# Kernel optimization log

Measured on AMD Instinct MI355X. Metric: run time of the kernel, lower is better.

The kernel has to match this reference:

```python
import jax, jax.numpy as jnp
import numpy as np


def setup_inputs() -> dict:
    key = jax.random.key(0)
    ks = jax.random.split(key, 7)
    N, C, sy, sx = 1024, 384, 7, 7
    Dm, Dc = 64, 64
    Dg = C + Dm + Dc  # 512, must match f_t_global
    return {
        "f_t_global": jax.random.normal(ks[0], (N, Dg), dtype=jnp.float32),
        "x_t_local": jax.random.normal(ks[1], (N, C, sy, sx), dtype=jnp.float32),
        "x_t_prev_local": jax.random.normal(ks[2], (N, C, sy, sx), dtype=jnp.float32),
        "m_t": jax.random.normal(ks[3], (N, Dm), dtype=jnp.float32),
        "m_t_prev": jax.random.normal(ks[4], (N, Dm), dtype=jnp.float32),
        "c_t": jax.random.normal(ks[5], (N, Dc), dtype=jnp.float32),
        "c_t_prev": jax.random.normal(ks[6], (N, Dc), dtype=jnp.float32),
    }


def _join(loc, m, c):
    # loc: [S, N, C]; m: [N, Dm]; c: [N, Dc] -> [S, N, C+Dm+Dc]
    S, N, _ = loc.shape
    mc = jnp.concatenate([m, c], axis=-1)  # [N, Dm+Dc]
    mc = jnp.broadcast_to(mc[None], (S, N, mc.shape[-1]))
    return jnp.concatenate([loc, mc], axis=-1)


def _mean_ce_diag(logits):
    # logits: [S, N, N]; labels = arange(N) for every s -> mean over s of CE
    logp = jax.nn.log_softmax(logits, axis=-1)
    diag = jnp.diagonal(logp, axis1=1, axis2=2)  # [S, N]
    return -jnp.mean(diag)  # mean over N (per-step CE) and over S (the /(sx*sy))


def reference(f_t_global, x_t_local, x_t_prev_local, m_t, m_t_prev, c_t, c_t_prev):
    N, C, sy, sx = x_t_prev_local.shape
    S = sy * sx
    # [N,C,sy,sx] -> [S,N,C] (spatial locations batched)
    prev = x_t_prev_local.reshape(N, C, S).transpose(2, 0, 1)
    cur = x_t_local.reshape(N, C, S).transpose(2, 0, 1)
    pos = _join(prev, m_t_prev, c_t_prev)   # [S, N, D]
    # loss1: global features vs per-location previous positives
    logits1 = jnp.einsum('id,sjd->sij', f_t_global, pos)  # [S, N, N]
    loss1 = _mean_ce_diag(logits1)
    # loss2: per-location current predictions vs previous positives
    pred2 = _join(cur, m_t, c_t)            # [S, N, D]
    logits2 = jnp.einsum('sid,sjd->sij', pred2, pos)
    loss2 = _mean_ce_diag(logits2)
    loss = loss1 + loss2
    return (loss, x_t_prev_local, x_t_local)
```

## Files before the change

kernel.cpp:

```cpp
#include <hip/hip_runtime.h>
#include <hip/hip_bf16.h>

typedef __attribute__((ext_vector_type(8))) __bf16 bf16x8;
typedef __attribute__((ext_vector_type(4))) float  f32x4;

#define SDIM 49
#define NDIM 1024
#define CDIM 384
#define DDIM 512
#define DMC  64
#define SCALE (1.0f/(SDIM*NDIM))
#define SLOT 65536

__device__ __forceinline__ void gload16(const void* g, void* l) {
    __builtin_amdgcn_global_load_lds((const __attribute__((address_space(1))) void*)g,
                                     (__attribute__((address_space(3))) void*)l, 16, 0, 0);
}

__global__ __launch_bounds__(512) void pack_copy_kernel(
    const float* __restrict__ xloc, const float* __restrict__ mv,
    const float* __restrict__ cv,   __hip_bfloat16* __restrict__ dst,
    float* __restrict__ cpy)
{
    const int j = blockIdx.x;
    const int d = threadIdx.x;
    float vals[SDIM];
    if (d < CDIM) {
        const float* p = xloc + ((size_t)j * CDIM + d) * SDIM;
        #pragma unroll
        for (int s = 0; s < SDIM; ++s) vals[s] = p[s];
        float* dcp = cpy + ((size_t)j * CDIM + d) * SDIM;
        #pragma unroll
        for (int s = 0; s < SDIM; ++s) dcp[s] = vals[s];
    } else if (d < CDIM + DMC) {
        float v = mv[j * DMC + (d - CDIM)];
        #pragma unroll
        for (int s = 0; s < SDIM; ++s) vals[s] = v;
    } else {
        float v = cv[j * DMC + (d - CDIM - DMC)];
        #pragma unroll
        for (int s = 0; s < SDIM; ++s) vals[s] = v;
    }
    #pragma unroll
    for (int s = 0; s < SDIM; ++s)
        dst[((size_t)s * NDIM + j) * DDIM + d] = __float2bfloat16(vals[s]);
}

__global__ void fpack_kernel(const float* __restrict__ f,
                             __hip_bfloat16* __restrict__ dst, int n)
{
    int i = blockIdx.x * blockDim.x + threadIdx.x;
    if (i < n) dst[i] = __float2bfloat16(f[i]);
}

__global__ __launch_bounds__(512, 2) void loss_kernel(
    const __hip_bfloat16* __restrict__ Fm,
    const __hip_bfloat16* __restrict__ Km,
    const __hip_bfloat16* __restrict__ Qm,
    float2* __restrict__ part,
    float* __restrict__ out)
{
    extern __shared__ __attribute__((aligned(16))) char sm[];

    const int bid = blockIdx.x;
    const int xcd = bid & 7;
    const int jj  = bid >> 3;
    const int g0  = 196 * xcd;
    const int gend = g0 + 196;

    const int tid  = threadIdx.x;
    const int lane = tid & 63;
    const int w    = tid >> 6;
    const int l15  = lane & 15;
    const int l4   = lane >> 4;
    const int wk   = w >> 2;
    const int wq   = w & 3;

    const int trow = tid >> 3;
    const int scol = (((tid & 7) ^ ((tid >> 3) & 7)) << 4);

    const unsigned xo   = (unsigned)((l15 & 7) << 4);
    const unsigned arow = (unsigned)((wk * 128 + l15) * 128);
    const unsigned brow = 32768u + (unsigned)((wq * 64 + l15) * 128);

    auto APtr = [&](int g) -> const char* {
        const int s = g >> 5, kb = (g >> 3) & 3;
        return (const char*)Km + ((size_t)s * NDIM + (size_t)kb * 256) * 1024;
    };
    auto BPtr = [&](int g) -> const char* {
        const int s = g >> 5, qb = g & 7;
        return (qb < 4)
            ? ((const char*)Fm + (size_t)qb * 256 * 1024)
            : ((const char*)Qm + ((size_t)s * NDIM + (size_t)(qb - 4) * 256) * 1024);
    };
    auto stage8 = [&](const char* A, const char* B, int ko, char* slot) {
        #pragma unroll
        for (int c = 0; c < 4; ++c) {
            gload16(A + (size_t)(c * 64 + trow) * 1024 + ko + scol,
                    slot + c * 8192 + tid * 16);
            gload16(B + (size_t)(c * 64 + trow) * 1024 + ko + scol,
                    slot + 32768 + c * 8192 + tid * 16);
        }
    };

    f32x4 acc[8][4];
    bf16x8 afr[8], bfr[4];

    #define READ12(KC) do {                                                   \
        const unsigned co = ((unsigned)((KC) * 64 + l4 * 16)) ^ xo;           \
        _Pragma("unroll")                                                     \
        for (int a = 0; a < 8; ++a)                                           \
            afr[a] = *(const bf16x8*)(sb_ + arow + a * 2048u + co);           \
        _Pragma("unroll")                                                     \
        for (int b = 0; b < 4; ++b)                                           \
            bfr[b] = *(const bf16x8*)(sb_ + brow + b * 2048u + co);           \
    } while (0)

    #define MFMA32() do {                                                     \
        _Pragma("unroll")                                                     \
        for (int a = 0; a < 8; ++a)                                           \
            _Pragma("unroll")                                                 \
            for (int b = 0; b < 4; ++b)                                       \
                acc[a][b] = __builtin_amdgcn_mfma_f32_16x16x32_bf16(          \
                    afr[a], bfr[b], acc[a][b], 0, 0, 0);                      \
    } while (0)

    stage8(APtr(g0 + jj), BPtr(g0 + jj), 0, sm);

    for (int g = g0 + jj; g < gend; g += 32) {
        const char* Ag = APtr(g);
        const char* Bg = BPtr(g);
        const bool hasNext = (g + 32) < gend;
        const char* An = hasNext ? APtr(g + 32) : Ag;
        const char* Bn = hasNext ? BPtr(g + 32) : Bg;

        #pragma unroll
        for (int a = 0; a < 8; ++a)
            #pragma unroll
            for (int b = 0; b < 4; ++b) acc[a][b] = f32x4{0.f, 0.f, 0.f, 0.f};

        #pragma unroll
        for (int t = 0; t < 8; ++t) {
            const char* sb_ = sm + (size_t)(t & 1) * SLOT;
            char* ns_ = sm + (size_t)((t + 1) & 1) * SLOT;

            __syncthreads();

            if ((t < 7) || hasNext) {
                const char* sA = (t < 7) ? Ag : An;
                const char* sB = (t < 7) ? Bg : Bn;
                stage8(sA, sB, (t < 7) ? (t + 1) * 128 : 0, ns_);
            }
            __builtin_amdgcn_sched_barrier(0);

            READ12(0);
            __builtin_amdgcn_s_setprio(1); MFMA32(); __builtin_amdgcn_s_setprio(0);
            READ12(1);
            __builtin_amdgcn_s_setprio(1); MFMA32(); __builtin_amdgcn_s_setprio(0);
        }

        const int s  = g >> 5;
        const int kb = (g >> 3) & 3;
        const int qb = g & 7;

        float q_m[4], q_s[4];
        #pragma unroll
        for (int b = 0; b < 4; ++b) {
            float m = -3.0e38f;
            #pragma unroll
            for (int a = 0; a < 8; ++a)
                #pragma unroll
                for (int r = 0; r < 4; ++r) m = fmaxf(m, acc[a][b][r]);
            float ss = 0.0f;
            #pragma unroll
            for (int a = 0; a < 8; ++a)
                #pragma unroll
                for (int r = 0; r < 4; ++r) ss += __expf(acc[a][b][r] - m);
            #pragma unroll
            for (int off = 16; off <= 32; off <<= 1) {
                float mo = __shfl_xor(m, off, 64);
                float so = __shfl_xor(ss, off, 64);
                float nm = fmaxf(m, mo);
                ss = ss * __expf(m - nm) + so * __expf(mo - nm);
                m = nm;
            }
            q_m[b] = m; q_s[b] = ss;
        }
        if (lane < 16) {
            const size_t rowb = (size_t)s * 2048 + (size_t)qb * 256 + wq * 64 + lane;
            #pragma unroll
            for (int b = 0; b < 4; ++b)
                part[(rowb + b * 16) * 8 + kb * 2 + wk] = make_float2(q_m[b], q_s[b]);
        }

        if (kb == (qb & 3) && (wq >> 1) == wk) {
            float d = 0.0f;
            const bool lok = (((lane >> 2) & 3) == l4);
            if (wq & 1) {
                #pragma unroll
                for (int b = 0; b < 4; ++b)
                    #pragma unroll
                    for (int r = 0; r < 4; ++r)
                        if (lok && r == (lane & 3)) d += acc[4 + b][b][r];
            } else {
                #pragma unroll
                for (int b = 0; b < 4; ++b)
                    #pragma unroll
                    for (int r = 0; r < 4; ++r)
                        if (lok && r == (lane & 3)) d += acc[b][b][r];
            }
            #pragma unroll
            for (int off = 1; off < 64; off <<= 1) d += __shfl_xor(d, off, 64);
            if (lane == 0) atomicAdd(out, -d * SCALE);
        }
    }
    #undef READ12
    #undef MFMA32
}

__global__ __launch_bounds__(256) void reduce_kernel(
    const float2* __restrict__ part, float* __restrict__ out)
{
    const int row = blockIdx.x * 256 + threadIdx.x;
    const float2* p = part + (size_t)row * 8;
    float m = -3.0e38f;
    float2 q[8];
    #pragma unroll
    for (int i = 0; i < 8; ++i) { q[i] = p[i]; m = fmaxf(m, q[i].x); }
    float ssum = 0.0f;
    #pragma unroll
    for (int i = 0; i < 8; ++i) ssum += q[i].y * __expf(q[i].x - m);
    float v = m + __logf(ssum);
    #pragma unroll
    for (int off = 1; off < 64; off <<= 1) v += __shfl_xor(v, off, 64);
    __shared__ float red[4];
    const int lane = threadIdx.x & 63, w = threadIdx.x >> 6;
    if (lane == 0) red[w] = v;
    __syncthreads();
    if (threadIdx.x == 0)
        atomicAdd(out, (red[0] + red[1] + red[2] + red[3]) * SCALE);
}

extern "C" void kernel_launch(void* const* d_in, const int* in_sizes, int n_in,
                              void* d_out, int out_size, void* d_ws, size_t ws_size,
                              hipStream_t stream)
{
    (void)in_sizes; (void)n_in; (void)out_size; (void)ws_size;
    const float* f  = (const float*)d_in[0];
    const float* x  = (const float*)d_in[1];
    const float* xp = (const float*)d_in[2];
    const float* mt = (const float*)d_in[3];
    const float* mp = (const float*)d_in[4];
    const float* ct = (const float*)d_in[5];
    const float* cp = (const float*)d_in[6];
    float* out = (float*)d_out;

    char* ws = (char*)d_ws;
    const size_t packBytes = (size_t)SDIM * NDIM * DDIM * 2;
    __hip_bfloat16* Km = (__hip_bfloat16*)ws;
    __hip_bfloat16* Qm = (__hip_bfloat16*)(ws + packBytes);
    __hip_bfloat16* Fm = (__hip_bfloat16*)(ws + 2 * packBytes);
    float2* part = (float2*)(ws + 2 * packBytes + (size_t)NDIM * DDIM * 2);

    hipMemsetAsync(out, 0, sizeof(float), stream);

    const int sz = NDIM * CDIM * SDIM;
    pack_copy_kernel<<<NDIM, 512, 0, stream>>>(xp, mp, cp, Km, out + 1);
    pack_copy_kernel<<<NDIM, 512, 0, stream>>>(x,  mt, ct, Qm, out + 1 + sz);
    fpack_kernel<<<(NDIM * DDIM + 255) / 256, 256, 0, stream>>>(f, Fm, NDIM * DDIM);

    loss_kernel<<<256, 512, 2 * SLOT, stream>>>(Fm, Km, Qm, part, out);
    reduce_kernel<<<392, 256, 0, stream>>>(part, out);
}
```

Before: 241.7 us.

## Precompute shared m/c logit contribution once and shrink GEMM K to 384

The m/c columns are identical across all spatial steps, so their contribution to both logits matrices is computed once by a new small MFMA kernel into two fp32 1024x1024 matrices. The main loss GEMM then loads its accumulators from these matrices and iterates over only the 384 local channels. Packed K/Q buffers shrink accordingly, which cuts pack-kernel write traffic and GEMM FLOPs by a quarter. The cost is an extra launch and fp32 reads of the precomputed matrix per tile.

After: 273.5 us. 1.13x slower.

```diff
diff --git a/kernel.cpp b/kernel.cpp
--- a/kernel.cpp
+++ b/kernel.cpp
@@ -7,8 +7,9 @@
 #define SDIM 49
 #define NDIM 1024
 #define CDIM 384
-#define DDIM 512
+#define KDIM 384
 #define DMC  64
+#define NSTEP 6
 #define SCALE (1.0f/(SDIM*NDIM))
 #define SLOT 65536
 
@@ -20,43 +21,99 @@
 __global__ __launch_bounds__(512) void pack_copy_kernel(
     const float* __restrict__ xloc, const float* __restrict__ mv,
     const float* __restrict__ cv,   __hip_bfloat16* __restrict__ dst,
-    float* __restrict__ cpy)
+    __hip_bfloat16* __restrict__ mcm, float* __restrict__ cpy)
 {
     const int j = blockIdx.x;
     const int d = threadIdx.x;
-    float vals[SDIM];
     if (d < CDIM) {
+        float vals[SDIM];
         const float* p = xloc + ((size_t)j * CDIM + d) * SDIM;
         #pragma unroll
         for (int s = 0; s < SDIM; ++s) vals[s] = p[s];
         float* dcp = cpy + ((size_t)j * CDIM + d) * SDIM;
         #pragma unroll
         for (int s = 0; s < SDIM; ++s) dcp[s] = vals[s];
-    } else if (d < CDIM + DMC) {
-        float v = mv[j * DMC + (d - CDIM)];
-        #pragma unroll
-        for (int s = 0; s < SDIM; ++s) vals[s] = v;
+        #pragma unroll
+        for (int s = 0; s < SDIM; ++s)
+            dst[((size_t)s * NDIM + j) * KDIM + d] = __float2bfloat16(vals[s]);
     } else {
-        float v = cv[j * DMC + (d - CDIM - DMC)];
-        #pragma unroll
-        for (int s = 0; s < SDIM; ++s) vals[s] = v;
+        const float v = (d < CDIM + DMC) ? mv[j * DMC + (d - CDIM)]
+                                         : cv[j * DMC + (d - CDIM - DMC)];
+        mcm[j * 128 + (d - CDIM)] = __float2bfloat16(v);
     }
-    #pragma unroll
-    for (int s = 0; s < SDIM; ++s)
-        dst[((size_t)s * NDIM + j) * DDIM + d] = __float2bfloat16(vals[s]);
 }
 
 __global__ void fpack_kernel(const float* __restrict__ f,
-                             __hip_bfloat16* __restrict__ dst, int n)
+                             __hip_bfloat16* __restrict__ Fm,
+                             __hip_bfloat16* __restrict__ fmc, int n)
 {
     int i = blockIdx.x * blockDim.x + threadIdx.x;
-    if (i < n) dst[i] = __float2bfloat16(f[i]);
+    if (i >= n) return;
+    const int r = i >> 9, d = i & 511;
+    const __hip_bfloat16 v = __float2bfloat16(f[i]);
+    if (d < CDIM) Fm[r * CDIM + d] = v;
+    else          fmc[r * 128 + (d - CDIM)] = v;
+}
+
+__global__ __launch_bounds__(256) void mker_kernel(
+    const __hip_bfloat16* __restrict__ fmc, const __hip_bfloat16* __restrict__ mct,
+    const __hip_bfloat16* __restrict__ mcp, float* __restrict__ M)
+{
+    const int bid = blockIdx.x;
+    const int qt = bid >> 3, kt = bid & 7;
+    const int tid = threadIdx.x, lane = tid & 63, wv = tid >> 6;
+    const int l15 = lane & 15, l4 = lane >> 4;
+    const int wk = wv >> 1, wq = wv & 1;
+
+    const char* Ab = (const char*)mcp;
+    const char* B1 = (const char*)fmc;
+    const char* B2 = (const char*)mct;
+
+    f32x4 acc1[4][4], acc2[4][4];
+    #pragma unroll
+    for (int a = 0; a < 4; ++a)
+        #pragma unroll
+        for (int b = 0; b < 4; ++b) { acc1[a][b] = f32x4{}; acc2[a][b] = f32x4{}; }
+
+    #pragma unroll
+    for (int kc = 0; kc < 4; ++kc) {
+        const int kco = kc * 64 + l4 * 16;
+        bf16x8 af[4], b1f[4], b2f[4];
+        #pragma unroll
+        for (int a = 0; a < 4; ++a) {
+            const int j = kt * 128 + wk * 64 + a * 16 + l15;
+            af[a] = *(const bf16x8*)(Ab + j * 256 + kco);
+        }
+        #pragma unroll
+        for (int b = 0; b < 4; ++b) {
+            const int i = qt * 128 + wq * 64 + b * 16 + l15;
+            b1f[b] = *(const bf16x8*)(B1 + i * 256 + kco);
+            b2f[b] = *(const bf16x8*)(B2 + i * 256 + kco);
+        }
+        #pragma unroll
+        for (int a = 0; a < 4; ++a)
+            #pragma unroll
+            for (int b = 0; b < 4; ++b) {
+                acc1[a][b] = __builtin_amdgcn_mfma_f32_16x16x32_bf16(af[a], b1f[b], acc1[a][b], 0, 0, 0);
+                acc2[a][b] = __builtin_amdgcn_mfma_f32_16x16x32_bf16(af[a], b2f[b], acc2[a][b], 0, 0, 0);
+            }
+    }
+    #pragma unroll
+    for (int a = 0; a < 4; ++a)
+        #pragma unroll
+        for (int b = 0; b < 4; ++b) {
+            const size_t q   = qt * 128 + wq * 64 + b * 16 + l15;
+            const size_t key = kt * 128 + wk * 64 + a * 16 + l4 * 4;
+            *(f32x4*)(M + (q << 10) + key) = acc1[a][b];
+            *(f32x4*)(M + (1u << 20) + (q << 10) + key) = acc2[a][b];
+        }
 }
 
 __global__ __launch_bounds__(512, 2) void loss_kernel(
     const __hip_bfloat16* __restrict__ Fm,
     const __hip_bfloat16* __restrict__ Km,
     const __hip_bfloat16* __restrict__ Qm,
+    const float* __restrict__ M,
     float2* __restrict__ part,
     float* __restrict__ out)
 {
@@ -85,20 +142,20 @@
 
     auto APtr = [&](int g) -> const char* {
         const int s = g >> 5, kb = (g >> 3) & 3;
-        return (const char*)Km + ((size_t)s * NDIM + (size_t)kb * 256) * 1024;
+        return (const char*)Km + ((size_t)s * NDIM + (size_t)kb * 256) * (KDIM * 2);
     };
     auto BPtr = [&](int g) -> const char* {
         const int s = g >> 5, qb = g & 7;
         return (qb < 4)
-            ? ((const char*)Fm + (size_t)qb * 256 * 1024)
-            : ((const char*)Qm + ((size_t)s * NDIM + (size_t)(qb - 4) * 256) * 1024);
+            ? ((const char*)Fm + (size_t)qb * 256 * (KDIM * 2))
+            : ((const char*)Qm + ((size_t)s * NDIM + (size_t)(qb - 4) * 256) * (KDIM * 2));
     };
     auto stage8 = [&](const char* A, const char* B, int ko, char* slot) {
         #pragma unroll
         for (int c = 0; c < 4; ++c) {
-            gload16(A + (size_t)(c * 64 + trow) * 1024 + ko + scol,
+            gload16(A + (size_t)(c * 64 + trow) * (KDIM * 2) + ko + scol,
                     slot + c * 8192 + tid * 16);
-            gload16(B + (size_t)(c * 64 + trow) * 1024 + ko + scol,
+            gload16(B + (size_t)(c * 64 + trow) * (KDIM * 2) + ko + scol,
                     slot + 32768 + c * 8192 + tid * 16);
         }
     };
@@ -134,22 +191,33 @@
         const char* An = hasNext ? APtr(g + 32) : Ag;
         const char* Bn = hasNext ? BPtr(g + 32) : Bg;
 
-        #pragma unroll
-        for (int a = 0; a < 8; ++a)
-            #pragma unroll
-            for (int b = 0; b < 4; ++b) acc[a][b] = f32x4{0.f, 0.f, 0.f, 0.f};
-
-        #pragma unroll
-        for (int t = 0; t < 8; ++t) {
+        const int s  = g >> 5;
+        const int kb = (g >> 3) & 3;
+        const int qb = g & 7;
+
+        {
+            const float* Mp = M + ((size_t)(qb >= 4) << 20);
+            const int qloc   = (qb & 3) * 256 + wq * 64 + l15;
+            const int keyloc = kb * 256 + wk * 128 + l4 * 4;
+            #pragma unroll
+            for (int a = 0; a < 8; ++a)
+                #pragma unroll
+                for (int b = 0; b < 4; ++b)
+                    acc[a][b] = *(const f32x4*)(Mp + ((size_t)(qloc + b * 16) << 10)
+                                                + keyloc + a * 16);
+        }
+
+        #pragma unroll
+        for (int t = 0; t < NSTEP; ++t) {
             const char* sb_ = sm + (size_t)(t & 1) * SLOT;
             char* ns_ = sm + (size_t)((t + 1) & 1) * SLOT;
 
             __syncthreads();
 
-            if ((t < 7) || hasNext) {
-                const char* sA = (t < 7) ? Ag : An;
-                const char* sB = (t < 7) ? Bg : Bn;
-                stage8(sA, sB, (t < 7) ? (t + 1) * 128 : 0, ns_);
+            if ((t < NSTEP - 1) || hasNext) {
+                const char* sA = (t < NSTEP - 1) ? Ag : An;
+                const char* sB = (t < NSTEP - 1) ? Bg : Bn;
+                stage8(sA, sB, (t < NSTEP - 1) ? (t + 1) * 128 : 0, ns_);
             }
             __builtin_amdgcn_sched_barrier(0);
 
@@ -158,10 +226,6 @@
             READ12(1);
             __builtin_amdgcn_s_setprio(1); MFMA32(); __builtin_amdgcn_s_setprio(0);
         }
-
-        const int s  = g >> 5;
-        const int kb = (g >> 3) & 3;
-        const int qb = g & 7;
 
         float q_m[4], q_s[4];
         #pragma unroll
@@ -256,19 +320,25 @@
     float* out = (float*)d_out;
 
     char* ws = (char*)d_ws;
-    const size_t packBytes = (size_t)SDIM * NDIM * DDIM * 2;
-    __hip_bfloat16* Km = (__hip_bfloat16*)ws;
-    __hip_bfloat16* Qm = (__hip_bfloat16*)(ws + packBytes);
-    __hip_bfloat16* Fm = (__hip_bfloat16*)(ws + 2 * packBytes);
-    float2* part = (float2*)(ws + 2 * packBytes + (size_t)NDIM * DDIM * 2);
+    const size_t packBytes = (size_t)SDIM * NDIM * KDIM * 2;
+    __hip_bfloat16* Km  = (__hip_bfloat16*)ws;
+    __hip_bfloat16* Qm  = (__hip_bfloat16*)(ws + packBytes);
+    char* p2 = ws + 2 * packBytes;
+    __hip_bfloat16* Fm  = (__hip_bfloat16*)p2;                 p2 += (size_t)NDIM * KDIM * 2;
+    __hip_bfloat16* fmc = (__hip_bfloat16*)p2;                 p2 += (size_t)NDIM * 128 * 2;
+    __hip_bfloat16* mcp = (__hip_bfloat16*)p2;                 p2 += (size_t)NDIM * 128 * 2;
+    __hip_bfloat16* mct = (__hip_bfloat16*)p2;                 p2 += (size_t)NDIM * 128 * 2;
+    float* M            = (float*)p2;                          p2 += (size_t)2 * NDIM * NDIM * 4;
+    float2* part        = (float2*)p2;
 
     hipMemsetAsync(out, 0, sizeof(float), stream);
 
     const int sz = NDIM * CDIM * SDIM;
-    pack_copy_kernel<<<NDIM, 512, 0, stream>>>(xp, mp, cp, Km, out + 1);
-    pack_copy_kernel<<<NDIM, 512, 0, stream>>>(x,  mt, ct, Qm, out + 1 + sz);
-    fpack_kernel<<<(NDIM * DDIM + 255) / 256, 256, 0, stream>>>(f, Fm, NDIM * DDIM);
-
-    loss_kernel<<<256, 512, 2 * SLOT, stream>>>(Fm, Km, Qm, part, out);
+    pack_copy_kernel<<<NDIM, 512, 0, stream>>>(xp, mp, cp, Km, mcp, out + 1);
+    pack_copy_kernel<<<NDIM, 512, 0, stream>>>(x,  mt, ct, Qm, mct, out + 1 + sz);
+    fpack_kernel<<<(NDIM * 512 + 255) / 256, 256, 0, stream>>>(f, Fm, fmc, NDIM * 512);
+    mker_kernel<<<64, 256, 0, stream>>>(fmc, mct, mcp, M);
+
+    loss_kernel<<<256, 512, 2 * SLOT, stream>>>(Fm, Km, Qm, M, part, out);
     reduce_kernel<<<392, 256, 0, stream>>>(part, out);
 }
```

## Switch packed operands to FP8 and use scaled 16x16x128 MFMA

Applied to the files above, without the earlier changes.

Packs K, Q and F into FP8 (e4m3) instead of bf16 and replaces the bf16 16x16x32 MFMA with the gfx950 scaled f8f6f4 16x16x128 MFMA. This halves the bytes written by the pack kernels and read by the GEMM, and halves the K-loop trip count, aiming to relieve both bandwidth and matrix-core cost. The risk is a large precision loss on logits from 512-dim dot products of normal inputs, which could push the loss outside tolerance.

Result: slower. 375.8 us (+55.5%).

```diff
diff --git a/kernel.cpp b/kernel.cpp
--- a/kernel.cpp
+++ b/kernel.cpp
@@ -1,14 +1,16 @@
 #include <hip/hip_runtime.h>
 #include <hip/hip_bf16.h>
 
-typedef __attribute__((ext_vector_type(8))) __bf16 bf16x8;
-typedef __attribute__((ext_vector_type(4))) float  f32x4;
+typedef __attribute__((ext_vector_type(8))) int   i32x8;
+typedef __attribute__((ext_vector_type(4))) int   i32x4;
+typedef __attribute__((ext_vector_type(4))) float f32x4;
 
 #define SDIM 49
 #define NDIM 1024
 #define CDIM 384
 #define DDIM 512
 #define DMC  64
+#define NSTEP 4
 #define SCALE (1.0f/(SDIM*NDIM))
 #define SLOT 65536
 
@@ -17,9 +19,13 @@
                                      (__attribute__((address_space(3))) void*)l, 16, 0, 0);
 }
 
+__device__ __forceinline__ unsigned char f2fp8(float v) {
+    return (unsigned char)(__builtin_amdgcn_cvt_pk_fp8_f32(v, v, 0, false) & 0xff);
+}
+
 __global__ __launch_bounds__(512) void pack_copy_kernel(
     const float* __restrict__ xloc, const float* __restrict__ mv,
-    const float* __restrict__ cv,   __hip_bfloat16* __restrict__ dst,
+    const float* __restrict__ cv,   unsigned char* __restrict__ dst,
     float* __restrict__ cpy)
 {
     const int j = blockIdx.x;
@@ -43,20 +49,20 @@
     }
     #pragma unroll
     for (int s = 0; s < SDIM; ++s)
-        dst[((size_t)s * NDIM + j) * DDIM + d] = __float2bfloat16(vals[s]);
+        dst[((size_t)s * NDIM + j) * DDIM + d] = f2fp8(vals[s]);
 }
 
 __global__ void fpack_kernel(const float* __restrict__ f,
-                             __hip_bfloat16* __restrict__ dst, int n)
+                             unsigned char* __restrict__ dst, int n)
 {
     int i = blockIdx.x * blockDim.x + threadIdx.x;
-    if (i < n) dst[i] = __float2bfloat16(f[i]);
+    if (i < n) dst[i] = f2fp8(f[i]);
 }
 
 __global__ __launch_bounds__(512, 2) void loss_kernel(
-    const __hip_bfloat16* __restrict__ Fm,
-    const __hip_bfloat16* __restrict__ Km,
-    const __hip_bfloat16* __restrict__ Qm,
+    const unsigned char* __restrict__ Fm,
+    const unsigned char* __restrict__ Km,
+    const unsigned char* __restrict__ Qm,
     float2* __restrict__ part,
     float* __restrict__ out)
 {
@@ -82,57 +88,57 @@
     const unsigned xo   = (unsigned)((l15 & 7) << 4);
     const unsigned arow = (unsigned)((wk * 128 + l15) * 128);
     const unsigned brow = 32768u + (unsigned)((wq * 64 + l15) * 128);
-
-    auto APtr = [&](int g) -> const char* {
+    const unsigned ko4  = (unsigned)(l4 * 32);
+
+    auto APtr = [&](int g) -> const unsigned char* {
         const int s = g >> 5, kb = (g >> 3) & 3;
-        return (const char*)Km + ((size_t)s * NDIM + (size_t)kb * 256) * 1024;
+        return Km + ((size_t)s * NDIM + (size_t)kb * 256) * DDIM;
     };
-    auto BPtr = [&](int g) -> const char* {
+    auto BPtr = [&](int g) -> const unsigned char* {
         const int s = g >> 5, qb = g & 7;
         return (qb < 4)
-            ? ((const char*)Fm + (size_t)qb * 256 * 1024)
-            : ((const char*)Qm + ((size_t)s * NDIM + (size_t)(qb - 4) * 256) * 1024);
+            ? (Fm + (size_t)qb * 256 * DDIM)
+            : (Qm + ((size_t)s * NDIM + (size_t)(qb - 4) * 256) * DDIM);
     };
-    auto stage8 = [&](const char* A, const char* B, int ko, char* slot) {
+    auto stage8 = [&](const unsigned char* A, const unsigned char* B, int ko, char* slot) {
         #pragma unroll
         for (int c = 0; c < 4; ++c) {
-            gload16(A + (size_t)(c * 64 + trow) * 1024 + ko + scol,
+            gload16(A + (size_t)(c * 64 + trow) * DDIM + ko + scol,
                     slot + c * 8192 + tid * 16);
-            gload16(B + (size_t)(c * 64 + trow) * 1024 + ko + scol,
+            gload16(B + (size_t)(c * 64 + trow) * DDIM + ko + scol,
                     slot + 32768 + c * 8192 + tid * 16);
         }
     };
 
     f32x4 acc[8][4];
-    bf16x8 afr[8], bfr[4];
-
-    #define READ12(KC) do {                                                   \
-        const unsigned co = ((unsigned)((KC) * 64 + l4 * 16)) ^ xo;           \
+    i32x8 afr[4], bfr[4];
+
+    #define LOADFRAG(D, BASE) do {                                            \
+        i32x4 lo_ = *(const i32x4*)(sb_ + (BASE) + (ko4 ^ xo));               \
+        i32x4 hi_ = *(const i32x4*)(sb_ + (BASE) + ((ko4 + 16u) ^ xo));       \
+        D[0]=lo_[0]; D[1]=lo_[1]; D[2]=lo_[2]; D[3]=lo_[3];                   \
+        D[4]=hi_[0]; D[5]=hi_[1]; D[6]=hi_[2]; D[7]=hi_[3];                   \
+    } while (0)
+
+    #define MFMA16(AH) do {                                                   \
         _Pragma("unroll")                                                     \
-        for (int a = 0; a < 8; ++a)                                           \
-            afr[a] = *(const bf16x8*)(sb_ + arow + a * 2048u + co);           \
-        _Pragma("unroll")                                                     \
-        for (int b = 0; b < 4; ++b)                                           \
-            bfr[b] = *(const bf16x8*)(sb_ + brow + b * 2048u + co);           \
-    } while (0)
-
-    #define MFMA32() do {                                                     \
-        _Pragma("unroll")                                                     \
-        for (int a = 0; a < 8; ++a)                                           \
+        for (int a = 0; a < 4; ++a)                                           \
             _Pragma("unroll")                                                 \
             for (int b = 0; b < 4; ++b)                                       \
-                acc[a][b] = __builtin_amdgcn_mfma_f32_16x16x32_bf16(          \
-                    afr[a], bfr[b], acc[a][b], 0, 0, 0);                      \
+                acc[(AH)*4 + a][b] =                                          \
+                    __builtin_amdgcn_mfma_scale_f32_16x16x128_f8f6f4(         \
+                        afr[a], bfr[b], acc[(AH)*4 + a][b],                   \
+                        0, 0, 0, 127, 0, 127);                                \
     } while (0)
 
     stage8(APtr(g0 + jj), BPtr(g0 + jj), 0, sm);
 
     for (int g = g0 + jj; g < gend; g += 32) {
-        const char* Ag = APtr(g);
-        const char* Bg = BPtr(g);
+        const unsigned char* Ag = APtr(g);
+        const unsigned char* Bg = BPtr(g);
         const bool hasNext = (g + 32) < gend;
-        const char* An = hasNext ? APtr(g + 32) : Ag;
-        const char* Bn = hasNext ? BPtr(g + 32) : Bg;
+        const unsigned char* An = hasNext ? APtr(g + 32) : Ag;
+        const unsigned char* Bn = hasNext ? BPtr(g + 32) : Bg;
 
         #pragma unroll
         for (int a = 0; a < 8; ++a)
@@ -140,23 +146,27 @@
             for (int b = 0; b < 4; ++b) acc[a][b] = f32x4{0.f, 0.f, 0.f, 0.f};
 
         #pragma unroll
-        for (int t = 0; t < 8; ++t) {
+        for (int t = 0; t < NSTEP; ++t) {
             const char* sb_ = sm + (size_t)(t & 1) * SLOT;
             char* ns_ = sm + (size_t)((t + 1) & 1) * SLOT;
 
             __syncthreads();
 
-            if ((t < 7) || hasNext) {
-                const char* sA = (t < 7) ? Ag : An;
-                const char* sB = (t < 7) ? Bg : Bn;
-                stage8(sA, sB, (t < 7) ? (t + 1) * 128 : 0, ns_);
+            if ((t < NSTEP - 1) || hasNext) {
+                const unsigned char* sA = (t < NSTEP - 1) ? Ag : An;
+                const unsigned char* sB = (t < NSTEP - 1) ? Bg : Bn;
+                stage8(sA, sB, (t < NSTEP - 1) ? (t + 1) * 128 : 0, ns_);
             }
             __builtin_amdgcn_sched_barrier(0);
 
-            READ12(0);
-            __builtin_amdgcn_s_setprio(1); MFMA32(); __builtin_amdgcn_s_setprio(0);
-            READ12(1);
-            __builtin_amdgcn_s_setprio(1); MFMA32(); __builtin_amdgcn_s_setprio(0);
+            #pragma unroll
+            for (int a = 0; a < 4; ++a) LOADFRAG(afr[a], arow + a * 2048u);
+            #pragma unroll
+            for (int b = 0; b < 4; ++b) LOADFRAG(bfr[b], brow + b * 2048u);
+            __builtin_amdgcn_s_setprio(1); MFMA16(0); __builtin_amdgcn_s_setprio(0);
+            #pragma unroll
+            for (int a = 0; a < 4; ++a) LOADFRAG(afr[a], arow + (4 + a) * 2048u);
+            __builtin_amdgcn_s_setprio(1); MFMA16(1); __builtin_amdgcn_s_setprio(0);
         }
 
         const int s  = g >> 5;
@@ -214,8 +224,8 @@
             if (lane == 0) atomicAdd(out, -d * SCALE);
         }
     }
-    #undef READ12
-    #undef MFMA32
+    #undef LOADFRAG
+    #undef MFMA16
 }
 
 __global__ __launch_bounds__(256) void reduce_kernel(
@@ -256,11 +266,11 @@
     float* out = (float*)d_out;
 
     char* ws = (char*)d_ws;
-    const size_t packBytes = (size_t)SDIM * NDIM * DDIM * 2;
-    __hip_bfloat16* Km = (__hip_bfloat16*)ws;
-    __hip_bfloat16* Qm = (__hip_bfloat16*)(ws + packBytes);
-    __hip_bfloat16* Fm = (__hip_bfloat16*)(ws + 2 * packBytes);
-    float2* part = (float2*)(ws + 2 * packBytes + (size_t)NDIM * DDIM * 2);
+    const size_t packBytes = (size_t)SDIM * NDIM * DDIM;
+    unsigned char* Km = (unsigned char*)ws;
+    unsigned char* Qm = (unsigned char*)(ws + packBytes);
+    unsigned char* Fm = (unsigned char*)(ws + 2 * packBytes);
+    float2* part = (float2*)(ws + 2 * packBytes + (size_t)NDIM * DDIM);
 
     hipMemsetAsync(out, 0, sizeof(float), stream);
 
```

## Move passthrough output copy into loss kernel epilogue to overlap with compute

Applied to the files above, without the earlier changes.

The fp32 copies of x_t_prev_local and x_t_local to the output are taken out of the pack kernels. Each loss-kernel tile now loads a 24576-float chunk into registers before its softmax epilogue and stores it afterwards, so the copy traffic overlaps with the epilogue math. The memset of the scalar loss is folded into the fpack kernel. This shortens the memory-bound pack kernels but adds 48 VGPRs of live state in the loss kernel and more memory traffic contending with the GEMM loads.

Result: faster. 221.1 us (-8.5%).

```diff
diff --git a/kernel.cpp b/kernel.cpp
--- a/kernel.cpp
+++ b/kernel.cpp
@@ -11,16 +11,16 @@
 #define DMC  64
 #define SCALE (1.0f/(SDIM*NDIM))
 #define SLOT 65536
+#define CHUNK 24576
 
 __device__ __forceinline__ void gload16(const void* g, void* l) {
     __builtin_amdgcn_global_load_lds((const __attribute__((address_space(1))) void*)g,
                                      (__attribute__((address_space(3))) void*)l, 16, 0, 0);
 }
 
-__global__ __launch_bounds__(512) void pack_copy_kernel(
+__global__ __launch_bounds__(512) void pack_kernel(
     const float* __restrict__ xloc, const float* __restrict__ mv,
-    const float* __restrict__ cv,   __hip_bfloat16* __restrict__ dst,
-    float* __restrict__ cpy)
+    const float* __restrict__ cv,   __hip_bfloat16* __restrict__ dst)
 {
     const int j = blockIdx.x;
     const int d = threadIdx.x;
@@ -29,9 +29,6 @@
         const float* p = xloc + ((size_t)j * CDIM + d) * SDIM;
         #pragma unroll
         for (int s = 0; s < SDIM; ++s) vals[s] = p[s];
-        float* dcp = cpy + ((size_t)j * CDIM + d) * SDIM;
-        #pragma unroll
-        for (int s = 0; s < SDIM; ++s) dcp[s] = vals[s];
     } else if (d < CDIM + DMC) {
         float v = mv[j * DMC + (d - CDIM)];
         #pragma unroll
@@ -47,9 +44,11 @@
 }
 
 __global__ void fpack_kernel(const float* __restrict__ f,
-                             __hip_bfloat16* __restrict__ dst, int n)
+                             __hip_bfloat16* __restrict__ dst, int n,
+                             float* __restrict__ out0)
 {
     int i = blockIdx.x * blockDim.x + threadIdx.x;
+    if (i == 0) out0[0] = 0.0f;
     if (i < n) dst[i] = __float2bfloat16(f[i]);
 }
 
@@ -57,6 +56,9 @@
     const __hip_bfloat16* __restrict__ Fm,
     const __hip_bfloat16* __restrict__ Km,
     const __hip_bfloat16* __restrict__ Qm,
+    const float* __restrict__ xp,
+    const float* __restrict__ xq,
+    float* __restrict__ outv,
     float2* __restrict__ part,
     float* __restrict__ out)
 {
@@ -163,6 +165,14 @@
         const int kb = (g >> 3) & 3;
         const int qb = g & 7;
 
+        const float* csrc = (g < 784) ? (xp + (size_t)g * CHUNK)
+                                      : (xq + (size_t)(g - 784) * CHUNK);
+        float* cdst = outv + (size_t)g * CHUNK;
+        f32x4 cbuf[12];
+        #pragma unroll
+        for (int i = 0; i < 12; ++i)
+            cbuf[i] = *(const f32x4*)(csrc + tid * 4 + i * 2048);
+
         float q_m[4], q_s[4];
         #pragma unroll
         for (int b = 0; b < 4; ++b) {
@@ -186,12 +196,6 @@
             }
             q_m[b] = m; q_s[b] = ss;
         }
-        if (lane < 16) {
-            const size_t rowb = (size_t)s * 2048 + (size_t)qb * 256 + wq * 64 + lane;
-            #pragma unroll
-            for (int b = 0; b < 4; ++b)
-                part[(rowb + b * 16) * 8 + kb * 2 + wk] = make_float2(q_m[b], q_s[b]);
-        }
 
         if (kb == (qb & 3) && (wq >> 1) == wk) {
             float d = 0.0f;
@@ -212,6 +216,17 @@
             #pragma unroll
             for (int off = 1; off < 64; off <<= 1) d += __shfl_xor(d, off, 64);
             if (lane == 0) atomicAdd(out, -d * SCALE);
+        }
+
+        #pragma unroll
+        for (int i = 0; i < 12; ++i)
+            *(f32x4*)(cdst + tid * 4 + i * 2048) = cbuf[i];
+
+        if (lane < 16) {
+            const size_t rowb = (size_t)s * 2048 + (size_t)qb * 256 + wq * 64 + lane;
+            #pragma unroll
+            for (int b = 0; b < 4; ++b)
+                part[(rowb + b * 16) * 8 + kb * 2 + wk] = make_float2(q_m[b], q_s[b]);
         }
     }
     #undef READ12
@@ -262,13 +277,10 @@
     __hip_bfloat16* Fm = (__hip_bfloat16*)(ws + 2 * packBytes);
     float2* part = (float2*)(ws + 2 * packBytes + (size_t)NDIM * DDIM * 2);
 
-    hipMemsetAsync(out, 0, sizeof(float), stream);
-
-    const int sz = NDIM * CDIM * SDIM;
-    pack_copy_kernel<<<NDIM, 512, 0, stream>>>(xp, mp, cp, Km, out + 1);
-    pack_copy_kernel<<<NDIM, 512, 0, stream>>>(x,  mt, ct, Qm, out + 1 + sz);
-    fpack_kernel<<<(NDIM * DDIM + 255) / 256, 256, 0, stream>>>(f, Fm, NDIM * DDIM);
-
-    loss_kernel<<<256, 512, 2 * SLOT, stream>>>(Fm, Km, Qm, part, out);
+    pack_kernel<<<NDIM, 512, 0, stream>>>(xp, mp, cp, Km);
+    pack_kernel<<<NDIM, 512, 0, stream>>>(x,  mt, ct, Qm);
+    fpack_kernel<<<(NDIM * DDIM + 255) / 256, 256, 0, stream>>>(f, Fm, NDIM * DDIM, out);
+
+    loss_kernel<<<256, 512, 2 * SLOT, stream>>>(Fm, Km, Qm, xp, x, out + 1, part, out);
     reduce_kernel<<<392, 256, 0, stream>>>(part, out);
 }
```
